# Kernel tuning notes

Measured on AMD Instinct MI355X. Metric: run time of the kernel, lower is better.

The kernel has to match this reference:

```python
import jax, jax.numpy as jnp
import numpy as np
import math

B, S, E, H = 4, 1024, 1024, 16
DH = E // H  # head dim = 64


def setup_inputs() -> dict:
    key = jax.random.key(0)
    ks = jax.random.split(key, 10)
    w_scale = math.sqrt(2.0 / (E + 3 * E))  # xavier-ish
    return {
        "x_real": jax.random.normal(ks[0], (B, S, E), jnp.float32),
        "x_imag": jax.random.normal(ks[1], (B, S, E), jnp.float32),
        "w_packed_real": jax.random.normal(ks[2], (3 * E, E), jnp.float32) * w_scale,
        "w_packed_imag": jax.random.normal(ks[3], (3 * E, E), jnp.float32) * w_scale,
        "b_packed_real": jax.random.normal(ks[4], (1, 3 * E), jnp.float32) * 0.02,
        "b_packed_imag": jax.random.normal(ks[5], (1, 3 * E), jnp.float32) * 0.02,
        "w_out_real": jax.random.normal(ks[6], (E, E), jnp.float32) * w_scale,
        "w_out_imag": jax.random.normal(ks[7], (E, E), jnp.float32) * w_scale,
        "b_out_real": jax.random.normal(ks[8], (1, E), jnp.float32) * 0.02,
        "b_out_imag": jax.random.normal(ks[9], (1, E), jnp.float32) * 0.02,
    }


def _to_c(r, i):
    return jax.lax.complex(r, i)


def _cmha(x, w_packed, b_packed, w_out, b_out):
    # packed QKV projection: x [B,S,E] @ W^T [E,3E] + b
    qkv = jnp.matmul(x, w_packed.T) + b_packed  # [B,S,3E]
    q, k, v = jnp.split(qkv, 3, axis=-1)  # each [B,S,E]
    # split heads -> [B,H,S,DH]
    split = lambda t: t.reshape(B, S, H, DH).transpose(0, 2, 1, 3)
    q, k, v = split(q), split(k), split(v)
    scale = 1.0 / math.sqrt(DH)
    scores = jnp.einsum("bhqd,bhkd->bhqk", q, k) * scale  # complex [B,H,S,S]
    # complex softmax: softmax over real and imag parts independently
    attn = jax.lax.complex(jax.nn.softmax(scores.real, axis=-1),
                           jax.nn.softmax(scores.imag, axis=-1))
    out = jnp.einsum("bhqk,bhkd->bhqd", attn, v)  # [B,H,S,DH]
    out = out.transpose(0, 2, 1, 3).reshape(B, S, E)
    return jnp.matmul(out, w_out.T) + b_out  # [B,S,E] complex


def reference(x_real, x_imag, w_packed_real, w_packed_imag, b_packed_real,
              b_packed_imag, w_out_real, w_out_imag, b_out_real, b_out_imag):
    x = _to_c(x_real, x_imag)
    w_packed = _to_c(w_packed_real, w_packed_imag)
    b_packed = _to_c(b_packed_real, b_packed_imag)
    w_out = _to_c(w_out_real, w_out_imag)
    b_out = _to_c(b_out_real, b_out_imag)
    return _cmha(x, w_packed, b_packed, w_out, b_out)
```

## Files before the change

### kernel.cpp

```cpp
#include <hip/hip_runtime.h>


typedef _Float16 f16;
typedef _Float16 f16x8 __attribute__((ext_vector_type(8)));
typedef _Float16 f16x4 __attribute__((ext_vector_type(4)));
typedef float f32x4 __attribute__((ext_vector_type(4)));
typedef float f32x16 __attribute__((ext_vector_type(16)));

#define MFMA16(a, b, c) __builtin_amdgcn_mfma_f32_16x16x32_f16(a, b, c, 0, 0, 0)
#define MFMA32(a, b, c) __builtin_amdgcn_mfma_f32_32x32x16_f16(a, b, c, 0, 0, 0)

__device__ inline void load_lds16(const void* g, void* l) {
  __builtin_amdgcn_global_load_lds(
      (const __attribute__((address_space(1))) unsigned int*)g,
      (__attribute__((address_space(3))) unsigned int*)l, 16, 0, 0);
}

__device__ inline unsigned pkrtz(float a, float b) {
  auto t = __builtin_amdgcn_cvt_pkrtz(a, b);
  return __builtin_bit_cast(unsigned, t);
}


__global__ void pack_x_kernel(const float* __restrict__ xr, const float* __restrict__ xi,
                              f16* __restrict__ XC) {
  int i = blockIdx.x * 256 + threadIdx.x;
  if (i >= (4096 * 2048 / 4)) return;
  int idx = i * 4;
  int m = idx >> 11, k = idx & 2047;
  const float* src = (k < 1024) ? (xr + (size_t)m * 1024 + k) : (xi + (size_t)m * 1024 + k - 1024);
  float4 v = *(const float4*)src;
  f16x4 o = {(f16)v.x, (f16)v.y, (f16)v.z, (f16)v.w};
  *(f16x4*)(XC + idx) = o;
}

__global__ void pack_wqkv_kernel(const float* __restrict__ wr, const float* __restrict__ wi,
                                 f16* __restrict__ W) {
  int i = blockIdx.x * 256 + threadIdx.x;
  if (i >= (6144 * 2048 / 4)) return;
  int idx = i * 4;
  int n = idx >> 11, k = idx & 2047;
  const float* base;
  float sgn = 1.f;
  if (n < 3072) {
    if (k < 1024) base = wr + (size_t)n * 1024 + k;
    else { base = wi + (size_t)n * 1024 + k - 1024; sgn = -1.f; }
  } else {
    int n2 = n - 3072;
    if (k < 1024) base = wi + (size_t)n2 * 1024 + k;
    else base = wr + (size_t)n2 * 1024 + k - 1024;
  }
  float4 v = *(const float4*)base;
  f16x4 o = {(f16)(sgn * v.x), (f16)(sgn * v.y), (f16)(sgn * v.z), (f16)(sgn * v.w)};
  *(f16x4*)(W + idx) = o;
}

__global__ void pack_wout_kernel(const float* __restrict__ wor, const float* __restrict__ woi,
                                 f16* __restrict__ W) {
  int i = blockIdx.x * 256 + threadIdx.x;
  if (i >= (2048 * 2048 / 4)) return;
  int idx = i * 4;
  int n = idx >> 11, k = idx & 2047;
  const float* base;
  float sgn = 1.f;
  if (n < 1024) {
    if (k < 1024) base = wor + (size_t)n * 1024 + k;
    else { base = woi + (size_t)n * 1024 + k - 1024; sgn = -1.f; }
  } else {
    int n2 = n - 1024;
    if (k < 1024) base = woi + (size_t)n2 * 1024 + k;
    else base = wor + (size_t)n2 * 1024 + k - 1024;
  }
  float4 v = *(const float4*)base;
  f16x4 o = {(f16)(sgn * v.x), (f16)(sgn * v.y), (f16)(sgn * v.z), (f16)(sgn * v.w)};
  *(f16x4*)(W + idx) = o;
}

struct GemmParams {
  f16 *QC, *KCr, *KCi, *VCT;
  const float *bpr, *bpi;
  float* out;
  const float *bor, *boi;
  int out_complex;
};


__global__ __launch_bounds__(256, 4) void gemm1_kernel(const f16* __restrict__ A,
                                                       const f16* __restrict__ B,
                                                       GemmParams p) {
  const int K = 2048;
  __shared__ alignas(16) f16 sA[2][128 * 32];
  __shared__ alignas(16) f16 sB[2][128 * 32];
  const int tid = threadIdx.x;
  const int w = tid >> 6, l = tid & 63;
  const int lr = l & 15, lk = l >> 4;
  const int lin = blockIdx.x;
  const int xcd = lin & 7, idx = lin >> 3;
  const int mt = idx / 6, ntl = idx % 6;
  const int tm0 = mt * 128;
  const int tn0 = (xcd * 6 + ntl) * 128;
  const int wm = (w >> 1) * 64, wn = (w & 1) * 64;

  const int srcC = ((tid & 3) ^ ((tid >> 3) & 3)) * 8;
  const f16* gA = A + (size_t)(tm0 + (tid >> 2)) * K + srcC;
  const f16* gB = B + (size_t)(tn0 + (tid >> 2)) * K + srcC;
  const int dst = w * 512;

#define STG(buf, k0) do {                                        \
    load_lds16(gA + (k0), &sA[buf][dst]);                        \
    load_lds16(gA + (size_t)64 * K + (k0), &sA[buf][2048 + dst]);\
    load_lds16(gB + (k0), &sB[buf][dst]);                        \
    load_lds16(gB + (size_t)64 * K + (k0), &sB[buf][2048 + dst]);\
  } while (0)

  f32x4 acc[4][4] = {};

  STG(0, 0);
  asm volatile("s_waitcnt vmcnt(0)" ::: "memory");
  __syncthreads();
  int cur = 0;

  for (int t = 0; t < 64; ++t) {
    if (t < 63) STG(cur ^ 1, (t + 1) * 32);
    f16x8 af[4], bf[4];
#pragma unroll
    for (int i = 0; i < 4; ++i) {
      int rowA = wm + i * 16 + lr;
      af[i] = *(const f16x8*)&sA[cur][rowA * 32 + (lk ^ ((rowA >> 1) & 3)) * 8];
      int rowB = wn + i * 16 + lr;
      bf[i] = *(const f16x8*)&sB[cur][rowB * 32 + (lk ^ ((rowB >> 1) & 3)) * 8];
    }
#pragma unroll
    for (int mi = 0; mi < 4; ++mi)
#pragma unroll
      for (int nj = 0; nj < 4; ++nj)
        acc[mi][nj] = MFMA16(af[mi], bf[nj], acc[mi][nj]);
    asm volatile("s_waitcnt vmcnt(0)" ::: "memory");
    __syncthreads();
    cur ^= 1;
  }
#undef STG

#pragma unroll
  for (int mi = 0; mi < 4; ++mi)
#pragma unroll
    for (int nj = 0; nj < 4; ++nj) {
      int n = tn0 + wn + nj * 16 + lr;
      bool im = n >= 3072;
      int nn = im ? n - 3072 : n;
      float bias = im ? p.bpi[nn] : p.bpr[nn];
      int part = nn >> 10;
      int e = nn & 1023, h = e >> 6, dd = e & 63;
      int m0 = tm0 + wm + mi * 16 + lk * 4;
      int bb = m0 >> 10, s0 = m0 & 1023;
      size_t bh = (size_t)bb * 16 + h;
      if (part == 0) {
#pragma unroll
        for (int r = 0; r < 4; ++r)
          p.QC[(bh * 1024 + s0 + r) * 128 + (im ? 64 : 0) + dd] =
              (f16)((acc[mi][nj][r] + bias) * 0.125f);
      } else if (part == 1) {
#pragma unroll
        for (int r = 0; r < 4; ++r) {
          float v2 = acc[mi][nj][r] + bias;
          size_t o = (bh * 1024 + s0 + r) * 128;
          if (!im) { p.KCr[o + dd] = (f16)v2; p.KCi[o + 64 + dd] = (f16)v2; }
          else     { p.KCr[o + 64 + dd] = (f16)(-v2); p.KCi[o + dd] = (f16)v2; }
        }
      } else {
        f16x4 vv;
#pragma unroll
        for (int r = 0; r < 4; ++r) vv[r] = (f16)(acc[mi][nj][r] + bias);
        *(f16x4*)&p.VCT[((bh * 128 + (im ? 64 : 0) + dd)) * 1024 + s0] = vv;
      }
    }
}


__global__ __launch_bounds__(256) void gemm_out_kernel(const f16* __restrict__ A,
                                                       const f16* __restrict__ B,
                                                       GemmParams p) {
  const int K = 2048;
  __shared__ alignas(16) f16 sA[128 * 64];
  __shared__ alignas(16) f16 sB[128 * 64];
  const int tid = threadIdx.x;
  const int w = tid >> 6, l = tid & 63;
  const int lr = l & 15, lk = l >> 4;
  const int nwg = gridDim.x * gridDim.y;
  const int lin = blockIdx.y * gridDim.x + blockIdx.x;
  const int qq = nwg >> 3, rr = nwg & 7;
  const int xcd = lin & 7, off = lin >> 3;
  const int swz = (xcd < rr ? xcd * (qq + 1) : rr * (qq + 1) + (xcd - rr) * qq) + off;
  const int tm0 = (swz / gridDim.x) * 128;
  const int tn0 = (swz % gridDim.x) * 128;
  const int wm = (w >> 1) * 64, wn = (w & 1) * 64;

  f32x4 acc[4][4] = {};

  for (int k0 = 0; k0 < K; k0 += 64) {
#pragma unroll
    for (int i = 0; i < 4; ++i) {
      int slot = i * 256 + tid;
      int row = slot >> 3;
      int cg = (slot & 7) ^ (row & 7);
      load_lds16(A + (size_t)(tm0 + row) * K + k0 + cg * 8, &sA[(size_t)(i * 256 + (w << 6)) * 8]);
      load_lds16(B + (size_t)(tn0 + row) * K + k0 + cg * 8, &sB[(size_t)(i * 256 + (w << 6)) * 8]);
    }
    __syncthreads();
#pragma unroll
    for (int kk = 0; kk < 2; ++kk) {
      f16x8 af[4], bf[4];
#pragma unroll
      for (int t = 0; t < 4; ++t) {
        int rowA = wm + t * 16 + lr;
        af[t] = *(const f16x8*)&sA[rowA * 64 + ((kk * 4 + lk) ^ (rowA & 7)) * 8];
        int rowB = wn + t * 16 + lr;
        bf[t] = *(const f16x8*)&sB[rowB * 64 + ((kk * 4 + lk) ^ (rowB & 7)) * 8];
      }
#pragma unroll
      for (int mt = 0; mt < 4; ++mt)
#pragma unroll
        for (int nt = 0; nt < 4; ++nt) acc[mt][nt] = MFMA16(af[mt], bf[nt], acc[mt][nt]);
    }
    __syncthreads();
  }

#pragma unroll
  for (int mt = 0; mt < 4; ++mt)
#pragma unroll
    for (int nt = 0; nt < 4; ++nt)
#pragma unroll
      for (int r = 0; r < 4; ++r) {
        int m = tm0 + wm + mt * 16 + lk * 4 + r;
        int n = tn0 + wn + nt * 16 + lr;
        float val = acc[mt][nt][r];
        if (n < 1024) {
          float v2 = val + p.bor[n];
          if (p.out_complex) p.out[((size_t)m * 1024 + n) * 2] = v2;
          else p.out[(size_t)m * 1024 + n] = v2;
        } else {
          if (p.out_complex) p.out[((size_t)m * 1024 + n - 1024) * 2 + 1] = val + p.boi[n - 1024];
        }
      }
}


__global__ __launch_bounds__(512, 2) void attn_kernel(const f16* __restrict__ QC,
                                                      const f16* __restrict__ KCr,
                                                      const f16* __restrict__ KCi,
                                                      const f16* __restrict__ VCT,
                                                      f16* __restrict__ OC) {
  __shared__ alignas(16) f16 sKr[2][32 * 128];
  __shared__ alignas(16) f16 sKi[2][32 * 128];
  __shared__ alignas(16) f16 sV[2][128 * 32];
  const int tid = threadIdx.x;
  const int w = tid >> 6, l = tid & 63;
  const int lq = l & 31, hi = l >> 5;
  const int bid = blockIdx.x;
  const int xx = bid & 7, yy = bid >> 3;
  const int bh = xx + ((yy >> 2) << 3);
  const int qt = yy & 3;
  const int q0 = qt * 256 + w * 32;
  const f16* Qb = QC + (size_t)bh * 1024 * 128;
  const f16* Krb = KCr + (size_t)bh * 1024 * 128;
  const f16* Kib = KCi + (size_t)bh * 1024 * 128;
  const f16* Vb = VCT + (size_t)bh * 128 * 1024;

  f16x8 qf[8];
#pragma unroll
  for (int c = 0; c < 8; ++c)
    qf[c] = *(const f16x8*)&Qb[(size_t)(q0 + lq) * 128 + c * 16 + hi * 8];

  f32x16 accR[4] = {};
  f32x16 accI[4] = {};
  float m_r = -1e30f, l_r = 0.f, m_i = -1e30f, l_i = 0.f;

  const int sprow = tid >> 3;
  const int cK = (tid & 7) ^ ((tid >> 4) & 7);
  const f16* gKr = Krb + (size_t)(tid >> 4) * 128 + ((tid >> 3) & 1) * 64 + cK * 8;
  const f16* gKi = Kib + (size_t)(tid >> 4) * 128 + ((tid >> 3) & 1) * 64 + cK * 8;
  const int cV = (tid & 7) ^ (sprow & 7);
  const f16* gV = Vb + (size_t)(sprow * 2 + (cV >> 2)) * 1024 + (cV & 3) * 8;
  const int ldsW = w * 512;

#define STAGE(s, k0)                                                 \
  do {                                                               \
    load_lds16(gKr + (size_t)(k0) * 128, &sKr[s][ldsW]);             \
    load_lds16(gKi + (size_t)(k0) * 128, &sKi[s][ldsW]);             \
    load_lds16(gV + (k0), &sV[s][ldsW]);                             \
  } while (0)

  STAGE(0, 0);
  asm volatile("s_waitcnt vmcnt(0)" ::: "memory");
  __syncthreads();
  int cur = 0;

  for (int t = 0; t < 32; ++t) {
    if (t < 31) STAGE(cur ^ 1, (t + 1) * 32);

    f32x16 sr = {}, si = {};
    __builtin_amdgcn_s_setprio(1);
#pragma unroll
    for (int c = 0; c < 8; ++c) {
      int fc = c * 2 + hi;
      int prow = lq * 2 + (fc >> 3);
      int swzc = (fc & 7) ^ (lq & 7);
      f16x8 kr = *(const f16x8*)&sKr[cur][prow * 64 + swzc * 8];
      f16x8 ki = *(const f16x8*)&sKi[cur][prow * 64 + swzc * 8];
      sr = MFMA32(kr, qf[c], sr);
      si = MFMA32(ki, qf[c], si);
    }
    __builtin_amdgcn_s_setprio(0);

    f16x8 prf[2], pif[2];
#pragma unroll
    for (int part = 0; part < 2; ++part) {
      const f32x16& s = part ? si : sr;
      float& m = part ? m_i : m_r;
      float& lsum = part ? l_i : l_r;
      f32x16* acc = part ? accI : accR;
      float vm = s[0];
#pragma unroll
      for (int j = 1; j < 16; ++j) vm = fmaxf(vm, s[j]);
      vm = fmaxf(vm, __shfl_xor(vm, 32));
      if (__any(vm > m + 8.f)) {
        float mn = fmaxf(m, vm);
        float sc = __expf(m - mn);
        lsum *= sc;
#pragma unroll
        for (int a = 0; a < 4; ++a)
#pragma unroll
          for (int j = 0; j < 16; ++j) acc[a][j] *= sc;
        m = mn;
      }
      float p[16];
      float ls = 0.f;
#pragma unroll
      for (int j = 0; j < 16; ++j) { p[j] = __expf(s[j] - m); ls += p[j]; }
      lsum += ls;
      unsigned a0 = pkrtz(p[0], p[1]), b0 = pkrtz(p[4], p[5]);
      unsigned a1 = pkrtz(p[2], p[3]), b1 = pkrtz(p[6], p[7]);
      unsigned a2 = pkrtz(p[8], p[9]), b2 = pkrtz(p[12], p[13]);
      unsigned a3 = pkrtz(p[10], p[11]), b3 = pkrtz(p[14], p[15]);
      asm("v_permlane32_swap_b32 %0, %1" : "+v"(a0), "+v"(b0));
      asm("v_permlane32_swap_b32 %0, %1" : "+v"(a1), "+v"(b1));
      asm("v_permlane32_swap_b32 %0, %1" : "+v"(a2), "+v"(b2));
      asm("v_permlane32_swap_b32 %0, %1" : "+v"(a3), "+v"(b3));
      union { unsigned u[4]; f16x8 v; } f0, f1;
      f0.u[0] = a0; f0.u[1] = a1; f0.u[2] = b0; f0.u[3] = b1;
      f1.u[0] = a2; f1.u[1] = a3; f1.u[2] = b2; f1.u[3] = b3;
      if (part) { pif[0] = f0.v; pif[1] = f1.v; }
      else      { prf[0] = f0.v; prf[1] = f1.v; }
    }

    __builtin_amdgcn_s_setprio(1);
#pragma unroll
    for (int ft = 0; ft < 4; ++ft) {
#pragma unroll
      for (int ks = 0; ks < 2; ++ks) {
        int feat = ft * 32 + lq;
        int prow = feat >> 1;
        int swzc = (((feat & 1) * 4 + ks * 2 + hi) ^ (prow & 7));
        f16x8 vf = *(const f16x8*)&sV[cur][prow * 64 + swzc * 8];
        accR[ft] = MFMA32(vf, prf[ks], accR[ft]);
        accI[ft] = MFMA32(vf, pif[ks], accI[ft]);
      }
    }
    __builtin_amdgcn_s_setprio(0);

    asm volatile("s_waitcnt vmcnt(0)" ::: "memory");
    __syncthreads();
    cur ^= 1;
  }
#undef STAGE

  float lr = l_r + __shfl_xor(l_r, 32);
  float li = l_i + __shfl_xor(l_i, 32);
  float ilr = 1.f / lr, ili = 1.f / li;
  const int bb = bh >> 4, h = bh & 15;
  const int q = q0 + lq;
  f16* rowp = OC + ((size_t)bb * 1024 + q) * 2048 + h * 64;
#pragma unroll
  for (int tt = 0; tt < 2; ++tt) {
#pragma unroll
    for (int g = 0; g < 4; ++g) {
      int d0 = tt * 32 + g * 8 + hi * 4;
      f16x4 ov, oiv;
#pragma unroll
      for (int j = 0; j < 4; ++j) {
        int rg = g * 4 + j;
        float orv = accR[tt][rg] * ilr - accI[tt + 2][rg] * ili;
        float oivv = accR[tt + 2][rg] * ilr + accI[tt][rg] * ili;
        ov[j] = (f16)orv;
        oiv[j] = (f16)oivv;
      }
      *(f16x4*)(rowp + d0) = ov;
      *(f16x4*)(rowp + 1024 + d0) = oiv;
    }
  }
}


extern "C" void kernel_launch(void* const* d_in, const int* in_sizes, int n_in,
                              void* d_out, int out_size, void* d_ws, size_t ws_size,
                              hipStream_t stream) {
  const float* xr = (const float*)d_in[0];
  const float* xi = (const float*)d_in[1];
  const float* wpr = (const float*)d_in[2];
  const float* wpi = (const float*)d_in[3];
  const float* bpr = (const float*)d_in[4];
  const float* bpi = (const float*)d_in[5];
  const float* wor = (const float*)d_in[6];
  const float* woi = (const float*)d_in[7];
  const float* bor = (const float*)d_in[8];
  const float* boi = (const float*)d_in[9];

  f16* ws = (f16*)d_ws;
  f16* XC = ws;
  f16* WQKV = XC + 8388608;
  f16* QC = WQKV + 12582912;
  f16* KCr = QC + 8388608;
  f16* KCi = KCr + 8388608;
  f16* VCT = KCi + 8388608;
  f16* OC = VCT + 8388608;
  f16* WOUT = OC + 8388608;

  pack_x_kernel<<<8192, 256, 0, stream>>>(xr, xi, XC);
  pack_wqkv_kernel<<<12288, 256, 0, stream>>>(wpr, wpi, WQKV);
  pack_wout_kernel<<<4096, 256, 0, stream>>>(wor, woi, WOUT);

  GemmParams p1 = {};
  p1.QC = QC; p1.KCr = KCr; p1.KCi = KCi; p1.VCT = VCT;
  p1.bpr = bpr; p1.bpi = bpi;
  gemm1_kernel<<<1536, 256, 0, stream>>>(XC, WQKV, p1);

  attn_kernel<<<256, 512, 0, stream>>>(QC, KCr, KCi, VCT, OC);

  GemmParams p2 = {};
  p2.out = (float*)d_out; p2.bor = bor; p2.boi = boi;
  p2.out_complex = (out_size == 8388608) ? 1 : 0;
  int ntilesN = p2.out_complex ? 16 : 8;
  gemm_out_kernel<<<dim3(ntilesN, 32), 256, 0, stream>>>(OC, WOUT, p2);
}
```

Baseline: 296.6 us.

## Enlarge QKV GEMM tile to 256x128 with split-phase LDS pipelining

Grows the QKV projection GEMM block tile from 128x128 to 256x128, giving each wave a 128x64 sub-tile, and halves the grid to 768 blocks. The K loop is split into two half-phases that interleave A/B global-to-LDS loads with MFMA work. It uses raw s_barrier, partial vmcnt waits and s_setprio to overlap loads with compute. The aim is more operand reuse per LDS read and fewer barriers per FLOP, at the cost of more registers, lower occupancy (launch bounds 4 to 2), and fragile hand-tuned synchronisation.

```diff
diff --git a/kernel.cpp b/kernel.cpp
--- a/kernel.cpp
+++ b/kernel.cpp
@@ -85,64 +85,98 @@
 };
 
 
-__global__ __launch_bounds__(256, 4) void gemm1_kernel(const f16* __restrict__ A,
+__global__ __launch_bounds__(256, 2) void gemm1_kernel(const f16* __restrict__ A,
                                                        const f16* __restrict__ B,
                                                        GemmParams p) {
   const int K = 2048;
-  __shared__ alignas(16) f16 sA[2][128 * 32];
-  __shared__ alignas(16) f16 sB[2][128 * 32];
+  __shared__ alignas(16) f16 sA[2][8192];
+  __shared__ alignas(16) f16 sB[2][4096];
   const int tid = threadIdx.x;
   const int w = tid >> 6, l = tid & 63;
   const int lr = l & 15, lk = l >> 4;
   const int lin = blockIdx.x;
   const int xcd = lin & 7, idx = lin >> 3;
   const int mt = idx / 6, ntl = idx % 6;
-  const int tm0 = mt * 128;
+  const int tm0 = mt * 256;
   const int tn0 = (xcd * 6 + ntl) * 128;
-  const int wm = (w >> 1) * 64, wn = (w & 1) * 64;
-
-  const int srcC = ((tid & 3) ^ ((tid >> 3) & 3)) * 8;
-  const f16* gA = A + (size_t)(tm0 + (tid >> 2)) * K + srcC;
-  const f16* gB = B + (size_t)(tn0 + (tid >> 2)) * K + srcC;
+  const int wm = (w >> 1) * 128, wn = (w & 1) * 64;
+
+  const int srow = tid >> 2;
+  const int sk8 = ((tid & 3) ^ ((tid >> 3) & 3)) * 8;
+  const f16* gA = A + (size_t)(tm0 + srow) * K + sk8;
+  const f16* gB = B + (size_t)(tn0 + srow) * K + sk8;
   const int dst = w * 512;
 
-#define STG(buf, k0) do {                                        \
-    load_lds16(gA + (k0), &sA[buf][dst]);                        \
-    load_lds16(gA + (size_t)64 * K + (k0), &sA[buf][2048 + dst]);\
-    load_lds16(gB + (k0), &sB[buf][dst]);                        \
-    load_lds16(gB + (size_t)64 * K + (k0), &sB[buf][2048 + dst]);\
+#define STGA(buf, k0) do {                                                    \
+    load_lds16(gA + (size_t)(k0), &sA[buf][dst]);                             \
+    load_lds16(gA + (size_t)64 * K + (size_t)(k0), &sA[buf][2048 + dst]);     \
+    load_lds16(gA + (size_t)128 * K + (size_t)(k0), &sA[buf][4096 + dst]);    \
+    load_lds16(gA + (size_t)192 * K + (size_t)(k0), &sA[buf][6144 + dst]);    \
   } while (0)
-
-  f32x4 acc[4][4] = {};
-
-  STG(0, 0);
+#define STGB(buf, k0) do {                                                    \
+    load_lds16(gB + (size_t)(k0), &sB[buf][dst]);                             \
+    load_lds16(gB + (size_t)64 * K + (size_t)(k0), &sB[buf][2048 + dst]);     \
+  } while (0)
+
+  f32x4 acc[8][4] = {};
+
+  STGA(0, 0);
+  STGB(0, 0);
+  STGA(1, 32);
   asm volatile("s_waitcnt vmcnt(0)" ::: "memory");
-  __syncthreads();
-  int cur = 0;
+  __builtin_amdgcn_s_barrier();
+
+  const int ca = (lk ^ ((lr >> 1) & 3)) * 8;
 
   for (int t = 0; t < 64; ++t) {
-    if (t < 63) STG(cur ^ 1, (t + 1) * 32);
-    f16x8 af[4], bf[4];
-#pragma unroll
-    for (int i = 0; i < 4; ++i) {
-      int rowA = wm + i * 16 + lr;
-      af[i] = *(const f16x8*)&sA[cur][rowA * 32 + (lk ^ ((rowA >> 1) & 3)) * 8];
-      int rowB = wn + i * 16 + lr;
-      bf[i] = *(const f16x8*)&sB[cur][rowB * 32 + (lk ^ ((rowB >> 1) & 3)) * 8];
-    }
-#pragma unroll
-    for (int mi = 0; mi < 4; ++mi)
-#pragma unroll
-      for (int nj = 0; nj < 4; ++nj)
+    const int buf = t & 1;
+    const f16* pA = &sA[buf][0];
+    const f16* pB = &sB[buf][0];
+    f16x8 af[8], bf[4];
+
+#pragma unroll
+    for (int mi = 0; mi < 8; ++mi)
+      af[mi] = *(const f16x8*)&pA[(wm + mi * 16 + lr) * 32 + ca];
+#pragma unroll
+    for (int nj = 0; nj < 2; ++nj)
+      bf[nj] = *(const f16x8*)&pB[(wn + nj * 16 + lr) * 32 + ca];
+    if (t < 63) STGB(buf ^ 1, (t + 1) * 32);
+    __builtin_amdgcn_s_barrier();
+    asm volatile("s_waitcnt lgkmcnt(0)" ::: "memory");
+    __builtin_amdgcn_sched_barrier(0);
+    __builtin_amdgcn_s_setprio(1);
+#pragma unroll
+    for (int mi = 0; mi < 8; ++mi)
+#pragma unroll
+      for (int nj = 0; nj < 2; ++nj)
         acc[mi][nj] = MFMA16(af[mi], bf[nj], acc[mi][nj]);
-    asm volatile("s_waitcnt vmcnt(0)" ::: "memory");
-    __syncthreads();
-    cur ^= 1;
-  }
-#undef STG
-
-#pragma unroll
-  for (int mi = 0; mi < 4; ++mi)
+    __builtin_amdgcn_s_setprio(0);
+    asm volatile("s_waitcnt vmcnt(4)" ::: "memory");
+    __builtin_amdgcn_s_barrier();
+
+#pragma unroll
+    for (int nj = 2; nj < 4; ++nj)
+      bf[nj] = *(const f16x8*)&pB[(wn + nj * 16 + lr) * 32 + ca];
+    if (t < 62) STGA(buf, (t + 2) * 32);
+    __builtin_amdgcn_s_barrier();
+    asm volatile("s_waitcnt lgkmcnt(0)" ::: "memory");
+    __builtin_amdgcn_sched_barrier(0);
+    __builtin_amdgcn_s_setprio(1);
+#pragma unroll
+    for (int mi = 0; mi < 8; ++mi)
+#pragma unroll
+      for (int nj = 2; nj < 4; ++nj)
+        acc[mi][nj] = MFMA16(af[mi], bf[nj], acc[mi][nj]);
+    __builtin_amdgcn_s_setprio(0);
+    if (t < 62) asm volatile("s_waitcnt vmcnt(4)" ::: "memory");
+    else asm volatile("s_waitcnt vmcnt(0)" ::: "memory");
+    __builtin_amdgcn_s_barrier();
+  }
+#undef STGA
+#undef STGB
+
+#pragma unroll
+  for (int mi = 0; mi < 8; ++mi)
 #pragma unroll
     for (int nj = 0; nj < 4; ++nj) {
       int n = tn0 + wn + nj * 16 + lr;
@@ -432,7 +466,7 @@
   GemmParams p1 = {};
   p1.QC = QC; p1.KCr = KCr; p1.KCi = KCi; p1.VCT = VCT;
   p1.bpr = bpr; p1.bpi = bpi;
-  gemm1_kernel<<<1536, 256, 0, stream>>>(XC, WQKV, p1);
+  gemm1_kernel<<<768, 256, 0, stream>>>(XC, WQKV, p1);
 
   attn_kernel<<<256, 512, 0, stream>>>(QC, KCr, KCi, VCT, OC);
 
```

Measured after the change: 306.4 us. +3.3%, slower.
